# Kernel optimization log

Measured on AMD Instinct MI355X. Metric: run time of the kernel, lower is better.

The kernel has to match this reference:

```python
import jax, jax.numpy as jnp
import numpy as np

B = 4096
MAX_ATOMS = 2048


def setup_inputs() -> dict:
    key = jax.random.key(0)
    k1, k2, k3 = jax.random.split(key, 3)
    coords_input = jax.random.normal(k1, (B, 3 * MAX_ATOMS), dtype=jnp.float32) * 10.0
    coords_target = jax.random.normal(k2, (B, 3 * MAX_ATOMS), dtype=jnp.float32) * 10.0
    num_atoms = jax.random.randint(k3, (B,), 64, MAX_ATOMS + 1, dtype=jnp.int32)
    return {"coords_input": coords_input, "coords_target": coords_target, "num_atoms": num_atoms}


def _kabsch_rmsd(coords_input, coords_target, num_atoms):
    b, f = coords_input.shape
    n_max = f // 3
    x = coords_input.reshape(b, n_max, 3)   # [B, N, 3] interleaved xyz per atom
    y = coords_target.reshape(b, n_max, 3)
    mask = (jnp.arange(n_max)[None, :] < num_atoms[:, None])[..., None]  # [B, N, 1]
    n = num_atoms.astype(x.dtype)[:, None, None]                          # [B, 1, 1]

    # masked centroids, then center and zero out padded atoms
    xm = jnp.where(mask, x, 0.0)
    ym = jnp.where(mask, y, 0.0)
    xc = (x - xm.sum(axis=1, keepdims=True) / n) * mask
    yc = (y - ym.sum(axis=1, keepdims=True) / n) * mask

    # 3x3 cross-covariance per batch element
    C = jnp.einsum('bni,bnj->bij', xc, yc)  # [B, 3, 3]
    s = jnp.linalg.svd(C, compute_uv=False)  # singular values, descending [B, 3]
    # Kabsch determinant correction: d = sign(det(U) det(V)) = sign(det(C))
    d = jnp.where(jnp.linalg.det(C) < 0.0, -1.0, 1.0).astype(x.dtype)
    trace = s[:, 0] + s[:, 1] + d * s[:, 2]

    gx = jnp.sum(xc * xc, axis=(1, 2))
    gy = jnp.sum(yc * yc, axis=(1, 2))
    msd = (gx + gy - 2.0 * trace) / jnp.squeeze(n, (1, 2))
    return jnp.sqrt(jnp.maximum(msd, 0.0))


def reference(coords_input, coords_target, num_atoms):
    return _kabsch_rmsd(coords_input, coords_target, num_atoms)
```

## Files before the change

### kernel.cpp

```cpp
#include <hip/hip_runtime.h>
#include <math.h>

#define N_MAX 2048
#define HALVES 2

#define ACC_ATOM(X0,X1,X2,Y0,Y1,Y2,M) do {                          \
    const float m_ = (M);                                           \
    const float x0 = (X0)*m_, x1 = (X1)*m_, x2 = (X2)*m_;           \
    const float y0 = (Y0)*m_, y1 = (Y1)*m_, y2 = (Y2)*m_;           \
    acc[0]  += x0;    acc[1]  += x1;    acc[2]  += x2;              \
    acc[3]  += y0;    acc[4]  += y1;    acc[5]  += y2;              \
    acc[6]  += x0*y0; acc[7]  += x0*y1; acc[8]  += x0*y2;           \
    acc[9]  += x1*y0; acc[10] += x1*y1; acc[11] += x1*y2;           \
    acc[12] += x2*y0; acc[13] += x2*y1; acc[14] += x2*y2;           \
    acc[15] += x0*x0 + x1*x1 + x2*x2;                               \
    acc[16] += y0*y0 + y1*y1 + y2*y2;                               \
} while (0)

__global__ __launch_bounds__(256) void kabsch_sums_kernel(
    const float* __restrict__ X, const float* __restrict__ Y,
    const int* __restrict__ num_atoms, float* __restrict__ ws, int B)
{
    const int wave = threadIdx.x >> 6;
    const int lane = threadIdx.x & 63;
    const int gw   = blockIdx.x * 4 + wave;
    const int b    = gw / HALVES;
    const int h    = gw % HALVES;
    if (b >= B) return;

    const int n  = num_atoms[b];
    const int nq = (n + 3) >> 2;

    const float4* __restrict__ x4 =
        reinterpret_cast<const float4*>(X + (size_t)b * (3 * N_MAX));
    const float4* __restrict__ y4 =
        reinterpret_cast<const float4*>(Y + (size_t)b * (3 * N_MAX));

    float acc[17];
#pragma unroll
    for (int i = 0; i < 17; ++i) acc[i] = 0.0f;

    for (int q = h * 64 + lane; q < nq; q += 64 * HALVES) {
        const int a0 = 4 * q;
        const int fi = 3 * q;
        const float4 xa = x4[fi + 0], xb = x4[fi + 1], xc = x4[fi + 2];
        const float4 ya = y4[fi + 0], yb = y4[fi + 1], yc = y4[fi + 2];
        const float m1 = (a0 + 1 < n) ? 1.0f : 0.0f;
        const float m2 = (a0 + 2 < n) ? 1.0f : 0.0f;
        const float m3 = (a0 + 3 < n) ? 1.0f : 0.0f;
        ACC_ATOM(xa.x, xa.y, xa.z, ya.x, ya.y, ya.z, 1.0f);
        ACC_ATOM(xa.w, xb.x, xb.y, ya.w, yb.x, yb.y, m1);
        ACC_ATOM(xb.z, xb.w, xc.x, yb.z, yb.w, yc.x, m2);
        ACC_ATOM(xc.y, xc.z, xc.w, yc.y, yc.z, yc.w, m3);
    }

#pragma unroll
    for (int i = 0; i < 17; ++i) {
#pragma unroll
        for (int off = 32; off > 0; off >>= 1)
            acc[i] += __shfl_down(acc[i], off);
    }

    if (lane == 0) {
#pragma unroll
        for (int i = 0; i < 17; ++i)
            ws[(size_t)(h * 17 + i) * B + b] = acc[i];
    }
}

__global__ __launch_bounds__(256) void kabsch_epilogue_kernel(
    const float* __restrict__ ws, const int* __restrict__ num_atoms,
    float* __restrict__ out, int B)
{
    const int b = blockIdx.x * 256 + threadIdx.x;
    if (b >= B) return;

    double s[17];
#pragma unroll
    for (int i = 0; i < 17; ++i) {
        double v = 0.0;
#pragma unroll
        for (int h = 0; h < HALVES; ++h)
            v += (double)ws[(size_t)(h * 17 + i) * B + b];
        s[i] = v;
    }

    const double dn = (double)num_atoms[b];
    const double Sx0 = s[0], Sx1 = s[1], Sx2 = s[2];
    const double Sy0 = s[3], Sy1 = s[4], Sy2 = s[5];

    double C[3][3];
    C[0][0] = s[6]  - Sx0 * Sy0 / dn;
    C[0][1] = s[7]  - Sx0 * Sy1 / dn;
    C[0][2] = s[8]  - Sx0 * Sy2 / dn;
    C[1][0] = s[9]  - Sx1 * Sy0 / dn;
    C[1][1] = s[10] - Sx1 * Sy1 / dn;
    C[1][2] = s[11] - Sx1 * Sy2 / dn;
    C[2][0] = s[12] - Sx2 * Sy0 / dn;
    C[2][1] = s[13] - Sx2 * Sy1 / dn;
    C[2][2] = s[14] - Sx2 * Sy2 / dn;

    const double gx = s[15] - (Sx0*Sx0 + Sx1*Sx1 + Sx2*Sx2) / dn;
    const double gy = s[16] - (Sy0*Sy0 + Sy1*Sy1 + Sy2*Sy2) / dn;

    const double det =
        C[0][0] * (C[1][1]*C[2][2] - C[1][2]*C[2][1]) -
        C[0][1] * (C[1][0]*C[2][2] - C[1][2]*C[2][0]) +
        C[0][2] * (C[1][0]*C[2][1] - C[1][1]*C[2][0]);

    double A00 = C[0][0]*C[0][0] + C[1][0]*C[1][0] + C[2][0]*C[2][0];
    double A11 = C[0][1]*C[0][1] + C[1][1]*C[1][1] + C[2][1]*C[2][1];
    double A22 = C[0][2]*C[0][2] + C[1][2]*C[1][2] + C[2][2]*C[2][2];
    double A01 = C[0][0]*C[0][1] + C[1][0]*C[1][1] + C[2][0]*C[2][1];
    double A02 = C[0][0]*C[0][2] + C[1][0]*C[1][2] + C[2][0]*C[2][2];
    double A12 = C[0][1]*C[0][2] + C[1][1]*C[1][2] + C[2][1]*C[2][2];

    double e0, e1, e2;
    const double q  = (A00 + A11 + A22) / 3.0;
    const double p1 = A01*A01 + A02*A02 + A12*A12;
    const double p2 = (A00-q)*(A00-q) + (A11-q)*(A11-q) + (A22-q)*(A22-q)
                      + 2.0 * p1;
    if (p2 <= 0.0) {
        e0 = e1 = e2 = q;
    } else {
        const double p = sqrt(p2 / 6.0);
        const double ip = 1.0 / p;
        const double b00 = (A00 - q) * ip, b11 = (A11 - q) * ip,
                     b22 = (A22 - q) * ip;
        const double b01 = A01 * ip, b02 = A02 * ip, b12 = A12 * ip;
        double r = 0.5 * (b00 * (b11*b22 - b12*b12)
                        - b01 * (b01*b22 - b12*b02)
                        + b02 * (b01*b12 - b11*b02));
        r = fmin(1.0, fmax(-1.0, r));
        const double phi = acos(r) / 3.0;
        e0 = q + 2.0 * p * cos(phi);
        e2 = q + 2.0 * p * cos(phi + 2.0943951023931953);
        e1 = 3.0 * q - e0 - e2;
    }

    const double s0 = sqrt(fmax(e0, 0.0));
    const double s1 = sqrt(fmax(e1, 0.0));
    const double s2 = sqrt(fmax(e2, 0.0));
    const double dsign = (det < 0.0) ? -1.0 : 1.0;
    const double trace = s0 + s1 + dsign * s2;

    const double msd = (gx + gy - 2.0 * trace) / dn;
    out[b] = (float)sqrt(fmax(msd, 0.0));
}

extern "C" void kernel_launch(void* const* d_in, const int* in_sizes, int n_in,
                              void* d_out, int out_size, void* d_ws, size_t ws_size,
                              hipStream_t stream) {
    const float* coords_input  = (const float*)d_in[0];
    const float* coords_target = (const float*)d_in[1];
    const int*   num_atoms     = (const int*)d_in[2];
    float* out = (float*)d_out;
    float* ws  = (float*)d_ws;

    const int B = out_size;
    const int waves = B * HALVES;
    const int blocksA = (waves + 3) / 4;
    kabsch_sums_kernel<<<blocksA, 256, 0, stream>>>(coords_input, coords_target,
                                                    num_atoms, ws, B);
    const int blocksB = (B + 255) / 256;
    kabsch_epilogue_kernel<<<blocksB, 256, 0, stream>>>(ws, num_atoms, out, B);
}
```

Before: 200.6 us.

## Split each batch row into four fixed atom segments with early exit

Each batch element is now handled by four waves, each covering a fixed 512-atom segment with at most two quad iterations per lane. Waves whose segment starts past num_atoms return immediately, so padded regions are never touched and work per wave stays short. The epilogue sums only the partial sums for segments that exist. Launching more waves raises memory-level parallelism, but the grid is larger, many waves do little, and the bounds check on b was dropped on the assumption that B is a multiple of one block.

After: 201.5 us, median of 2. Within noise of the previous version (+0.4%).

```diff
diff --git a/kernel.cpp b/kernel.cpp
--- a/kernel.cpp
+++ b/kernel.cpp
@@ -2,7 +2,9 @@
 #include <math.h>
 
 #define N_MAX 2048
-#define HALVES 2
+#define SEG 4
+#define SEG_ATOMS 512
+#define SEG_QUADS 128
 
 #define ACC_ATOM(X0,X1,X2,Y0,Y1,Y2,M) do {                          \
     const float m_ = (M);                                           \
@@ -17,6 +19,20 @@
     acc[16] += y0*y0 + y1*y1 + y2*y2;                               \
 } while (0)
 
+#define ACC_QUAD(Q) do {                                            \
+    const int a0 = 4 * (Q);                                         \
+    const int fi = 3 * (Q);                                         \
+    const float4 xa = x4[fi + 0], xb = x4[fi + 1], xc = x4[fi + 2]; \
+    const float4 ya = y4[fi + 0], yb = y4[fi + 1], yc = y4[fi + 2]; \
+    const float m1 = (a0 + 1 < n) ? 1.0f : 0.0f;                    \
+    const float m2 = (a0 + 2 < n) ? 1.0f : 0.0f;                    \
+    const float m3 = (a0 + 3 < n) ? 1.0f : 0.0f;                    \
+    ACC_ATOM(xa.x, xa.y, xa.z, ya.x, ya.y, ya.z, 1.0f);             \
+    ACC_ATOM(xa.w, xb.x, xb.y, ya.w, yb.x, yb.y, m1);               \
+    ACC_ATOM(xb.z, xb.w, xc.x, yb.z, yb.w, yc.x, m2);               \
+    ACC_ATOM(xc.y, xc.z, xc.w, yc.y, yc.z, yc.w, m3);               \
+} while (0)
+
 __global__ __launch_bounds__(256) void kabsch_sums_kernel(
     const float* __restrict__ X, const float* __restrict__ Y,
     const int* __restrict__ num_atoms, float* __restrict__ ws, int B)
@@ -24,13 +40,12 @@
     const int wave = threadIdx.x >> 6;
     const int lane = threadIdx.x & 63;
     const int gw   = blockIdx.x * 4 + wave;
-    const int b    = gw / HALVES;
-    const int h    = gw % HALVES;
-    if (b >= B) return;
+    const int b    = gw >> 2;
+    const int s    = gw & 3;
+    const int n    = num_atoms[b];
+    if (s * SEG_ATOMS >= n) return;
 
-    const int n  = num_atoms[b];
     const int nq = (n + 3) >> 2;
-
     const float4* __restrict__ x4 =
         reinterpret_cast<const float4*>(X + (size_t)b * (3 * N_MAX));
     const float4* __restrict__ y4 =
@@ -40,19 +55,10 @@
 #pragma unroll
     for (int i = 0; i < 17; ++i) acc[i] = 0.0f;
 
-    for (int q = h * 64 + lane; q < nq; q += 64 * HALVES) {
-        const int a0 = 4 * q;
-        const int fi = 3 * q;
-        const float4 xa = x4[fi + 0], xb = x4[fi + 1], xc = x4[fi + 2];
-        const float4 ya = y4[fi + 0], yb = y4[fi + 1], yc = y4[fi + 2];
-        const float m1 = (a0 + 1 < n) ? 1.0f : 0.0f;
-        const float m2 = (a0 + 2 < n) ? 1.0f : 0.0f;
-        const float m3 = (a0 + 3 < n) ? 1.0f : 0.0f;
-        ACC_ATOM(xa.x, xa.y, xa.z, ya.x, ya.y, ya.z, 1.0f);
-        ACC_ATOM(xa.w, xb.x, xb.y, ya.w, yb.x, yb.y, m1);
-        ACC_ATOM(xb.z, xb.w, xc.x, yb.z, yb.w, yc.x, m2);
-        ACC_ATOM(xc.y, xc.z, xc.w, yc.y, yc.z, yc.w, m3);
-    }
+    const int q0 = s * SEG_QUADS + lane;
+    if (q0 < nq)      ACC_QUAD(q0);
+    const int q1 = q0 + 64;
+    if (q1 < nq)      ACC_QUAD(q1);
 
 #pragma unroll
     for (int i = 0; i < 17; ++i) {
@@ -64,7 +70,7 @@
     if (lane == 0) {
 #pragma unroll
         for (int i = 0; i < 17; ++i)
-            ws[(size_t)(h * 17 + i) * B + b] = acc[i];
+            ws[(size_t)(s * 17 + i) * B + b] = acc[i];
     }
 }
 
@@ -75,17 +81,19 @@
     const int b = blockIdx.x * 256 + threadIdx.x;
     if (b >= B) return;
 
+    const int n    = num_atoms[b];
+    const int nseg = (n + SEG_ATOMS - 1) >> 9;
+
     double s[17];
 #pragma unroll
-    for (int i = 0; i < 17; ++i) {
-        double v = 0.0;
+    for (int i = 0; i < 17; ++i) s[i] = 0.0;
+    for (int h = 0; h < nseg; ++h) {
 #pragma unroll
-        for (int h = 0; h < HALVES; ++h)
-            v += (double)ws[(size_t)(h * 17 + i) * B + b];
-        s[i] = v;
+        for (int i = 0; i < 17; ++i)
+            s[i] += (double)ws[(size_t)(h * 17 + i) * B + b];
     }
 
-    const double dn = (double)num_atoms[b];
+    const double dn = (double)n;
     const double Sx0 = s[0], Sx1 = s[1], Sx2 = s[2];
     const double Sy0 = s[3], Sy1 = s[4], Sy2 = s[5];
 
@@ -158,8 +166,7 @@
     float* ws  = (float*)d_ws;
 
     const int B = out_size;
-    const int waves = B * HALVES;
-    const int blocksA = (waves + 3) / 4;
+    const int blocksA = B * SEG / 4;
     kabsch_sums_kernel<<<blocksA, 256, 0, stream>>>(coords_input, coords_target,
                                                     num_atoms, ws, B);
     const int blocksB = (B + 255) / 256;
```
